# Kernel tuning notes

Hardware: AMD Instinct MI355X
Metric: run time of the kernel (lower is better)

Reference implementation:

```python
import jax, jax.numpy as jnp
import numpy as np

B, C, H, W = 16, 64, 64, 64
MID = max(1, C // 8)


def setup_inputs() -> dict:
    key = jax.random.key(0)
    k1, k2, k3, k4, k5 = jax.random.split(key, 5)
    x = jax.random.normal(k1, (B, C, H, W), dtype=jnp.float32)
    # 1x1 conv weights (spectral-norm conv collapses to a plain [out,in] matrix
    # with a scalar-normalized weight; we use the effective weight directly)
    Wq = jax.random.normal(k2, (MID, C), dtype=jnp.float32) * 0.05
    Wk = jax.random.normal(k3, (MID, C), dtype=jnp.float32) * 0.05
    Wv = jax.random.normal(k4, (C, C), dtype=jnp.float32) * 0.05
    gamma = jax.random.normal(k5, (1,), dtype=jnp.float32) * 0.1
    return {"x": x, "Wq": Wq, "Wk": Wk, "Wv": Wv, "gamma": gamma}


def reference(x, Wq, Wk, Wv, gamma):
    b, c, h, w = x.shape
    n = h * w
    mid = Wq.shape[0]
    xf = x.reshape(b, c, n)                      # [B,C,N]
    q = jnp.einsum('mc,bcn->bnm', Wq, xf)        # [B,N,mid]
    k = jnp.einsum('mc,bcn->bmn', Wk, xf)        # [B,mid,N]
    scale = np.float32(1.0 / np.sqrt(mid))       # torch: / q.size(-1)**0.5, q last dim = mid
    attn = jax.nn.softmax(jnp.einsum('bnm,bmk->bnk', q, k) * scale, axis=-1)  # [B,N,N]
    v = jnp.einsum('oc,bcn->bon', Wv, xf)        # [B,C,N]
    # torch: bmm(v, attn^T) -> out[b,c,j] = sum_n v[b,c,n] * attn[b,j,n]
    out = jnp.einsum('bon,bjn->boj', v, attn).reshape(b, c, h, w)
    return gamma * out + x
```

## Files before the change

### kernel.cpp

```cpp
#include <hip/hip_runtime.h>
#include <hip/hip_bf16.h>

#define BATCH 16
#define CC    64
#define NN    4096
#define MIDD  8

typedef __attribute__((ext_vector_type(8)))  short short8;
typedef __attribute__((ext_vector_type(16))) float f32x16;
typedef __attribute__((ext_vector_type(2)))  int   v2i;

static __device__ __forceinline__ ushort f2bf(float f) {
    return __bfloat16_as_ushort(__float2bfloat16(f));
}

static __device__ __forceinline__ void glds16(const void* g, void* l) {
    __builtin_amdgcn_global_load_lds(
        (const __attribute__((address_space(1))) unsigned int*)g,
        (__attribute__((address_space(3))) unsigned int*)l, 16, 0, 0);
}

static __device__ __forceinline__ unsigned cvt_pk(float lo, float hi) {
    unsigned r;
    asm("v_cvt_pk_bf16_f32 %0, %1, %2" : "=v"(r) : "v"(lo), "v"(hi));
    return r;
}

__global__ __launch_bounds__(256) void proj_kernel(
    const float* __restrict__ x,
    const float* __restrict__ Wq,
    const float* __restrict__ Wk,
    const float* __restrict__ Wv,
    ushort* __restrict__ qtr,
    ushort* __restrict__ ktr,
    ushort* __restrict__ v)
{
    __shared__ unsigned xT[64 * 32];

    int tid = threadIdx.x;
    int b   = blockIdx.x >> 6;
    int n0  = (blockIdx.x & 63) * 64;

    {
        int n  = tid & 63;
        int cp = tid >> 6;
        const float* xb = x + (size_t)b * CC * NN + n0 + n;
#pragma unroll
        for (int rep = 0; rep < 8; ++rep) {
            int c = cp * 2 + rep * 8;
            float a0 = xb[(size_t)c * NN];
            float a1 = xb[(size_t)(c + 1) * NN];
            int dwlog = cp + rep * 4;
            xT[n * 32 + (dwlog ^ (n & 31))] = cvt_pk(a0, a1);
        }
    }

    int wv   = tid >> 6;
    int lane = tid & 63;
    int hi   = lane >> 5;
    int r    = lane & 31;
    int s_   = wv & 1;
    bool hiT = wv >= 2;

    short8 wfa[4], wfb[4];
    if (!hiT) {
        const float* r0 = (r < 8)  ? (Wq + r * 64)
                        : (r < 16) ? (Wk + (r - 8) * 64)
                                   : (Wv + (r - 16) * 64);
        const float* r1 = Wv + (16 + r) * 64;
#pragma unroll
        for (int kc = 0; kc < 4; ++kc) {
            const float4* p0 = (const float4*)(r0 + kc * 16 + hi * 8);
            const float4* p1 = (const float4*)(r1 + kc * 16 + hi * 8);
            float4 a = p0[0], c4 = p0[1];
            float4 e = p1[0], g4 = p1[1];
            union { short8 s8; unsigned u[4]; } wa, wb;
            wa.u[0] = cvt_pk(a.x, a.y);  wa.u[1] = cvt_pk(a.z, a.w);
            wa.u[2] = cvt_pk(c4.x, c4.y); wa.u[3] = cvt_pk(c4.z, c4.w);
            wb.u[0] = cvt_pk(e.x, e.y);  wb.u[1] = cvt_pk(e.z, e.w);
            wb.u[2] = cvt_pk(g4.x, g4.y); wb.u[3] = cvt_pk(g4.z, g4.w);
            wfa[kc] = wa.s8; wfb[kc] = wb.s8;
        }
    } else {
        const float* r2 = Wv + (size_t)(r < 16 ? (48 + r) : 48) * 64;
        short8 z8 = {};
#pragma unroll
        for (int kc = 0; kc < 4; ++kc) {
            const float4* p2 = (const float4*)(r2 + kc * 16 + hi * 8);
            float4 a = p2[0], c4 = p2[1];
            union { short8 s8; unsigned u[4]; } wa;
            wa.u[0] = cvt_pk(a.x, a.y);  wa.u[1] = cvt_pk(a.z, a.w);
            wa.u[2] = cvt_pk(c4.x, c4.y); wa.u[3] = cvt_pk(c4.z, c4.w);
            wfa[kc] = (r < 16) ? wa.s8 : z8;
            wfb[kc] = z8;
        }
    }

    __syncthreads();

    short8 bf[4];
    int nr = s_ * 32 + r;
#pragma unroll
    for (int kc = 0; kc < 4; ++kc) {
        union { short8 s8; unsigned u[4]; } bu;
#pragma unroll
        for (int i = 0; i < 4; ++i) {
            int dwlog = kc * 8 + hi * 4 + i;
            bu.u[i] = xT[nr * 32 + (dwlog ^ r)];
        }
        bf[kc] = bu.s8;
    }

    int ng = n0 + s_ * 32 + r;
    size_t nb = (size_t)b * NN + ng;
    const float SCLQ = 0.35355339059327373f * 1.4426950408889634f;

    if (!hiT) {
        f32x16 acc = {};
#pragma unroll
        for (int kc = 0; kc < 4; ++kc)
            acc = __builtin_amdgcn_mfma_f32_32x32x16_bf16(wfa[kc], bf[kc], acc, 0, 0, 0);
        uint2 qd, kd, zd; zd.x = 0; zd.y = 0;
        qd.x = cvt_pk(acc[0] * SCLQ, acc[1] * SCLQ);
        qd.y = cvt_pk(acc[2] * SCLQ, acc[3] * SCLQ);
        kd.x = cvt_pk(acc[4], acc[5]);
        kd.y = cvt_pk(acc[6], acc[7]);
        *(uint2*)(qtr + nb * 8 + hi * 4) = qd;
        *(uint2*)(ktr + nb * 16 + hi * 4) = kd;
        *(uint2*)(ktr + nb * 16 + 8 + hi * 4) = zd;
#pragma unroll
        for (int reg = 8; reg < 16; ++reg) {
            int ch = (reg & 3) + 8 * ((reg >> 2) - 2) + 4 * hi;
            v[((size_t)b * CC + ch) * NN + ng] = f2bf(acc[reg]);
        }
        f32x16 ac1 = {};
#pragma unroll
        for (int kc = 0; kc < 4; ++kc)
            ac1 = __builtin_amdgcn_mfma_f32_32x32x16_bf16(wfb[kc], bf[kc], ac1, 0, 0, 0);
#pragma unroll
        for (int reg = 0; reg < 16; ++reg) {
            int ch = 16 + (reg & 3) + 8 * (reg >> 2) + 4 * hi;
            v[((size_t)b * CC + ch) * NN + ng] = f2bf(ac1[reg]);
        }
    } else {
        f32x16 acc = {};
#pragma unroll
        for (int kc = 0; kc < 4; ++kc)
            acc = __builtin_amdgcn_mfma_f32_32x32x16_bf16(wfa[kc], bf[kc], acc, 0, 0, 0);
#pragma unroll
        for (int reg = 0; reg < 8; ++reg) {
            int ch = 48 + (reg & 3) + 8 * (reg >> 2) + 4 * hi;
            v[((size_t)b * CC + ch) * NN + ng] = f2bf(acc[reg]);
        }
    }
}

__global__ __launch_bounds__(256, 2) void attn_kernel(
    const ushort* __restrict__ qtr,
    const ushort* __restrict__ ktr,
    const ushort* __restrict__ v,
    const float*  __restrict__ x,
    const float*  __restrict__ gamma,
    float* __restrict__ out)
{
    __shared__ __align__(16) char lds[3 * 10240];

    int bid = blockIdx.x;
    int wg  = (bid & 7) * 64 + (bid >> 3);
    int b   = wg >> 5;
    int qt  = wg & 31;

    int tid  = threadIdx.x;
    int wv   = tid >> 6;
    int lane = tid & 63;
    int hi   = lane >> 5;
    int ql   = lane & 31;
    int q0   = qt * 128 + wv * 32;

    short8 qf = *(const short8*)(qtr + ((size_t)b * NN + q0 + ql) * 8);
    float  gm = gamma[0];
    short8 zero8 = {};
    if (hi) qf = zero8;
    asm volatile("s_waitcnt vmcnt(0)" ::: "memory");

    const ushort* kb_ = ktr + (size_t)b * NN * 16;
    const ushort* vb_ = v   + (size_t)b * CC * NN;

    int oA = tid >> 3, sA = (tid & 7) ^ (oA & 7);
    int oB = oA + 32,  sB = (tid & 7) ^ (oB & 7);
    const ushort* vsrcA = vb_ + (size_t)oA * NN + sA * 8;
    const ushort* vsrcB = vb_ + (size_t)oB * NN + sB * 8;
    const ushort* ksrc0 = kb_ + (size_t)(tid & 63) * 16 + (tid >> 6) * 8;
    int vdA = tid * 16, vdB = (tid + 256) * 16, kd_ = 8192 + tid * 16;

    char* b0 = lds;
    char* b1 = lds + 10240;
    char* b2 = lds + 20480;

    union { short8 s8; ushort us[8]; } onesu;
#pragma unroll
    for (int i = 0; i < 8; ++i) onesu.us[i] = 0x3F80;
    short8 ones = onesu.s8;

    f32x16 zf   = {};
    f32x16 acc0 = {};
    f32x16 acc1 = {};
    f32x16 accl = {};

    glds16(vsrcA, b0 + vdA); glds16(vsrcB, b0 + vdB);
    if (wv < 2) glds16(ksrc0, b0 + kd_);
    glds16(vsrcA + 64, b1 + vdA); glds16(vsrcB + 64, b1 + vdB);
    if (wv < 2) glds16(ksrc0 + 64 * 16, b1 + kd_);

    for (int t = 0; t < 64; ++t) {
        int k2 = ((t + 2) & 63) * 64;

        __builtin_amdgcn_s_barrier();
        glds16(vsrcA + k2, b2 + vdA);
        glds16(vsrcB + k2, b2 + vdB);
        if (wv < 2) {
            glds16(ksrc0 + (size_t)k2 * 16, b2 + kd_);
            asm volatile("s_waitcnt vmcnt(6)" ::: "memory");
        } else {
            asm volatile("s_waitcnt vmcnt(4)" ::: "memory");
        }
        __builtin_amdgcn_s_barrier();
        __builtin_amdgcn_sched_barrier(0);

        short8 kf0 = *(const short8*)(b0 + 8192 + (hi * 64 + ql) * 16);
        short8 kf1 = *(const short8*)(b0 + 8192 + (hi * 64 + 32 + ql) * 16);

        short8 vA[2][2], vB[2][2];
#pragma unroll
        for (int c = 0; c < 2; ++c)
#pragma unroll
            for (int f = 0; f < 2; ++f) {
                int byteA = (ql * 8 + ((c * 4 + f * 2 + hi) ^ (ql & 7))) * 16;
                vA[c][f] = *(const short8*)(b0 + byteA);
                vB[c][f] = *(const short8*)(b0 + byteA + 4096);
            }

        f32x16 s0 = __builtin_amdgcn_mfma_f32_32x32x16_bf16(kf0, qf, zf, 0, 0, 0);
        f32x16 s1 = __builtin_amdgcn_mfma_f32_32x32x16_bf16(kf1, qf, zf, 0, 0, 0);

#pragma unroll
        for (int c = 0; c < 2; ++c) {
            const f32x16& s = c ? s1 : s0;
            float p[16];
#pragma unroll
            for (int r = 0; r < 16; ++r) p[r] = __builtin_amdgcn_exp2f(s[r]);

            unsigned u[8];
#pragma unroll
            for (int i = 0; i < 8; ++i) u[i] = cvt_pk(p[2 * i], p[2 * i + 1]);

            v2i r02 = __builtin_amdgcn_permlane32_swap(u[0], u[2], false, false);
            v2i r13 = __builtin_amdgcn_permlane32_swap(u[1], u[3], false, false);
            v2i r46 = __builtin_amdgcn_permlane32_swap(u[4], u[6], false, false);
            v2i r57 = __builtin_amdgcn_permlane32_swap(u[5], u[7], false, false);
            union { short8 s8; int i4[4]; } P0, P1;
            P0.i4[0] = r02.x; P0.i4[1] = r13.x; P0.i4[2] = r02.y; P0.i4[3] = r13.y;
            P1.i4[0] = r46.x; P1.i4[1] = r57.x; P1.i4[2] = r46.y; P1.i4[3] = r57.y;

            __builtin_amdgcn_s_setprio(1);
            acc0 = __builtin_amdgcn_mfma_f32_32x32x16_bf16(vA[c][0], P0.s8, acc0, 0, 0, 0);
            acc1 = __builtin_amdgcn_mfma_f32_32x32x16_bf16(vB[c][0], P0.s8, acc1, 0, 0, 0);
            accl = __builtin_amdgcn_mfma_f32_32x32x16_bf16(ones,    P0.s8, accl, 0, 0, 0);
            acc0 = __builtin_amdgcn_mfma_f32_32x32x16_bf16(vA[c][1], P1.s8, acc0, 0, 0, 0);
            acc1 = __builtin_amdgcn_mfma_f32_32x32x16_bf16(vB[c][1], P1.s8, acc1, 0, 0, 0);
            accl = __builtin_amdgcn_mfma_f32_32x32x16_bf16(ones,    P1.s8, accl, 0, 0, 0);
            __builtin_amdgcn_s_setprio(0);
        }

        char* tp = b0; b0 = b1; b1 = b2; b2 = tp;
    }

    float inv = gm / accl[0];

#pragma unroll
    for (int r = 0; r < 16; ++r) {
        int o = (r & 3) + 8 * (r >> 2) + 4 * hi;
        size_t i0 = ((size_t)(b * CC + o)) * NN + q0 + ql;
        out[i0] = acc0[r] * inv + x[i0];
        size_t i1 = i0 + (size_t)32 * NN;
        out[i1] = acc1[r] * inv + x[i1];
    }
}

extern "C" void kernel_launch(void* const* d_in, const int* in_sizes, int n_in,
                              void* d_out, int out_size, void* d_ws, size_t ws_size,
                              hipStream_t stream) {
    const float* x     = (const float*)d_in[0];
    const float* Wq    = (const float*)d_in[1];
    const float* Wk    = (const float*)d_in[2];
    const float* Wv    = (const float*)d_in[3];
    const float* gamma = (const float*)d_in[4];
    float* out = (float*)d_out;

    ushort* qtr = (ushort*)d_ws;
    ushort* ktr = qtr + (size_t)BATCH * NN * 8;
    ushort* vws = ktr + (size_t)BATCH * NN * 16;

    proj_kernel<<<dim3((BATCH * NN) / 64), dim3(256), 0, stream>>>(x, Wq, Wk, Wv, qtr, ktr, vws);
    attn_kernel<<<dim3((BATCH * NN) / 128), dim3(256), 0, stream>>>(qtr, ktr, vws, x, gamma, out);
}
```

Measured before the change: 144.3 us.

## Split attention key range across two wave groups with LDS reduction

Doubles the workgroup to 512 threads, with two halves of four waves each processing half of the key sequence for the same query tile, each using its own triple-buffered LDS region. Partial numerators and denominators from the second half are combined through LDS before the first half writes the output. K fragment loads are re-swizzled to avoid LDS bank conflicts, and V/K fragment reads are moved next to their use to reduce register pressure. This raises wave count per CU, at the cost of an extra reduction pass, a doubled LDS footprint, and a higher occupancy target of four blocks.

```diff
diff --git a/kernel.cpp b/kernel.cpp
--- a/kernel.cpp
+++ b/kernel.cpp
@@ -155,7 +155,7 @@
     }
 }
 
-__global__ __launch_bounds__(256, 2) void attn_kernel(
+__global__ __launch_bounds__(512, 4) void attn_kernel(
     const ushort* __restrict__ qtr,
     const ushort* __restrict__ ktr,
     const ushort* __restrict__ v,
@@ -163,7 +163,7 @@
     const float*  __restrict__ gamma,
     float* __restrict__ out)
 {
-    __shared__ __align__(16) char lds[3 * 10240];
+    __shared__ __align__(16) char lds[2 * 3 * 10240];
 
     int bid = blockIdx.x;
     int wg  = (bid & 7) * 64 + (bid >> 3);
@@ -172,10 +172,13 @@
 
     int tid  = threadIdx.x;
     int wv   = tid >> 6;
+    int qs   = wv & 3;
+    int h    = wv >> 2;
     int lane = tid & 63;
     int hi   = lane >> 5;
     int ql   = lane & 31;
-    int q0   = qt * 128 + wv * 32;
+    int q0   = qt * 128 + qs * 32;
+    int gt   = tid & 255;
 
     short8 qf = *(const short8*)(qtr + ((size_t)b * NN + q0 + ql) * 8);
     float  gm = gamma[0];
@@ -183,19 +186,26 @@
     if (hi) qf = zero8;
     asm volatile("s_waitcnt vmcnt(0)" ::: "memory");
 
-    const ushort* kb_ = ktr + (size_t)b * NN * 16;
-    const ushort* vb_ = v   + (size_t)b * CC * NN;
-
-    int oA = tid >> 3, sA = (tid & 7) ^ (oA & 7);
-    int oB = oA + 32,  sB = (tid & 7) ^ (oB & 7);
-    const ushort* vsrcA = vb_ + (size_t)oA * NN + sA * 8;
-    const ushort* vsrcB = vb_ + (size_t)oB * NN + sB * 8;
-    const ushort* ksrc0 = kb_ + (size_t)(tid & 63) * 16 + (tid >> 6) * 8;
-    int vdA = tid * 16, vdB = (tid + 256) * 16, kd_ = 8192 + tid * 16;
-
-    char* b0 = lds;
-    char* b1 = lds + 10240;
-    char* b2 = lds + 20480;
+    const ushort* kbh = ktr + (size_t)b * NN * 16 + (size_t)h * 2048 * 16;
+    const ushort* vbh = v   + (size_t)b * CC * NN + h * 2048;
+
+    int oA = gt >> 3, sA = (gt & 7) ^ (oA & 7);
+    int oB = oA + 32,  sB = (gt & 7) ^ (oB & 7);
+    const ushort* vsrcA = vbh + (size_t)oA * NN + sA * 8;
+    const ushort* vsrcB = vbh + (size_t)oB * NN + sB * 8;
+    int lk = gt ^ ((gt >> 3) & 7);
+    const ushort* ksrc0 = kbh + (size_t)(lk >> 1) * 16 + (lk & 1) * 8;
+
+    char* base = lds + h * 30720;
+    int vdA = gt * 16, vdB = (gt + 256) * 16, kd_ = 8192 + gt * 16;
+    char* b0 = base;
+    char* b1 = base + 10240;
+    char* b2 = base + 20480;
+
+    int L0 = ql * 2 + hi;
+    int L1 = (32 + ql) * 2 + hi;
+    int k0off = 8192 + (L0 ^ ((L0 >> 3) & 7)) * 16;
+    int k1off = 8192 + (L1 ^ ((L1 >> 3) & 7)) * 16;
 
     union { short8 s8; ushort us[8]; } onesu;
 #pragma unroll
@@ -208,17 +218,17 @@
     f32x16 accl = {};
 
     glds16(vsrcA, b0 + vdA); glds16(vsrcB, b0 + vdB);
-    if (wv < 2) glds16(ksrc0, b0 + kd_);
+    if (gt < 128) glds16(ksrc0, b0 + kd_);
     glds16(vsrcA + 64, b1 + vdA); glds16(vsrcB + 64, b1 + vdB);
-    if (wv < 2) glds16(ksrc0 + 64 * 16, b1 + kd_);
-
-    for (int t = 0; t < 64; ++t) {
-        int k2 = ((t + 2) & 63) * 64;
+    if (gt < 128) glds16(ksrc0 + 64 * 16, b1 + kd_);
+
+    for (int t = 0; t < 32; ++t) {
+        int k2 = ((t + 2) & 31) * 64;
 
         __builtin_amdgcn_s_barrier();
         glds16(vsrcA + k2, b2 + vdA);
         glds16(vsrcB + k2, b2 + vdB);
-        if (wv < 2) {
+        if (gt < 128) {
             glds16(ksrc0 + (size_t)k2 * 16, b2 + kd_);
             asm volatile("s_waitcnt vmcnt(6)" ::: "memory");
         } else {
@@ -227,25 +237,11 @@
         __builtin_amdgcn_s_barrier();
         __builtin_amdgcn_sched_barrier(0);
 
-        short8 kf0 = *(const short8*)(b0 + 8192 + (hi * 64 + ql) * 16);
-        short8 kf1 = *(const short8*)(b0 + 8192 + (hi * 64 + 32 + ql) * 16);
-
-        short8 vA[2][2], vB[2][2];
-#pragma unroll
-        for (int c = 0; c < 2; ++c)
-#pragma unroll
-            for (int f = 0; f < 2; ++f) {
-                int byteA = (ql * 8 + ((c * 4 + f * 2 + hi) ^ (ql & 7))) * 16;
-                vA[c][f] = *(const short8*)(b0 + byteA);
-                vB[c][f] = *(const short8*)(b0 + byteA + 4096);
-            }
-
-        f32x16 s0 = __builtin_amdgcn_mfma_f32_32x32x16_bf16(kf0, qf, zf, 0, 0, 0);
-        f32x16 s1 = __builtin_amdgcn_mfma_f32_32x32x16_bf16(kf1, qf, zf, 0, 0, 0);
-
 #pragma unroll
         for (int c = 0; c < 2; ++c) {
-            const f32x16& s = c ? s1 : s0;
+            short8 kf = *(const short8*)(b0 + (c ? k1off : k0off));
+            f32x16 s = __builtin_amdgcn_mfma_f32_32x32x16_bf16(kf, qf, zf, 0, 0, 0);
+
             float p[16];
 #pragma unroll
             for (int r = 0; r < 16; ++r) p[r] = __builtin_amdgcn_exp2f(s[r]);
@@ -262,28 +258,53 @@
             P0.i4[0] = r02.x; P0.i4[1] = r13.x; P0.i4[2] = r02.y; P0.i4[3] = r13.y;
             P1.i4[0] = r46.x; P1.i4[1] = r57.x; P1.i4[2] = r46.y; P1.i4[3] = r57.y;
 
+            int g0 = (ql * 8 + ((c * 4 + hi) ^ (ql & 7))) * 16;
+            int g1 = (ql * 8 + ((c * 4 + 2 + hi) ^ (ql & 7))) * 16;
+            short8 vA0 = *(const short8*)(b0 + g0);
+            short8 vB0 = *(const short8*)(b0 + g0 + 4096);
+            short8 vA1 = *(const short8*)(b0 + g1);
+            short8 vB1 = *(const short8*)(b0 + g1 + 4096);
+
             __builtin_amdgcn_s_setprio(1);
-            acc0 = __builtin_amdgcn_mfma_f32_32x32x16_bf16(vA[c][0], P0.s8, acc0, 0, 0, 0);
-            acc1 = __builtin_amdgcn_mfma_f32_32x32x16_bf16(vB[c][0], P0.s8, acc1, 0, 0, 0);
-            accl = __builtin_amdgcn_mfma_f32_32x32x16_bf16(ones,    P0.s8, accl, 0, 0, 0);
-            acc0 = __builtin_amdgcn_mfma_f32_32x32x16_bf16(vA[c][1], P1.s8, acc0, 0, 0, 0);
-            acc1 = __builtin_amdgcn_mfma_f32_32x32x16_bf16(vB[c][1], P1.s8, acc1, 0, 0, 0);
-            accl = __builtin_amdgcn_mfma_f32_32x32x16_bf16(ones,    P1.s8, accl, 0, 0, 0);
+            acc0 = __builtin_amdgcn_mfma_f32_32x32x16_bf16(vA0, P0.s8, acc0, 0, 0, 0);
+            acc1 = __builtin_amdgcn_mfma_f32_32x32x16_bf16(vB0, P0.s8, acc1, 0, 0, 0);
+            accl = __builtin_amdgcn_mfma_f32_32x32x16_bf16(ones, P0.s8, accl, 0, 0, 0);
+            acc0 = __builtin_amdgcn_mfma_f32_32x32x16_bf16(vA1, P1.s8, acc0, 0, 0, 0);
+            acc1 = __builtin_amdgcn_mfma_f32_32x32x16_bf16(vB1, P1.s8, acc1, 0, 0, 0);
+            accl = __builtin_amdgcn_mfma_f32_32x32x16_bf16(ones, P1.s8, accl, 0, 0, 0);
             __builtin_amdgcn_s_setprio(0);
         }
 
         char* tp = b0; b0 = b1; b1 = b2; b2 = tp;
     }
 
-    float inv = gm / accl[0];
-
-#pragma unroll
-    for (int r = 0; r < 16; ++r) {
-        int o = (r & 3) + 8 * (r >> 2) + 4 * hi;
-        size_t i0 = ((size_t)(b * CC + o)) * NN + q0 + ql;
-        out[i0] = acc0[r] * inv + x[i0];
-        size_t i1 = i0 + (size_t)32 * NN;
-        out[i1] = acc1[r] * inv + x[i1];
+    asm volatile("s_waitcnt vmcnt(0)" ::: "memory");
+    __syncthreads();
+
+    float* cl = (float*)lds;
+    if (h == 1) {
+#pragma unroll
+        for (int r = 0; r < 16; ++r) {
+            int ch = (r & 3) + 8 * (r >> 2) + 4 * hi;
+            cl[(qs * 64 + ch) * 32 + ql]      = acc0[r];
+            cl[(qs * 64 + 32 + ch) * 32 + ql] = acc1[r];
+        }
+        cl[8192 + qs * 32 + ql] = accl[0];
+    }
+    __syncthreads();
+    if (h == 0) {
+        float den = accl[0] + cl[8192 + qs * 32 + ql];
+        float inv = gm / den;
+#pragma unroll
+        for (int r = 0; r < 16; ++r) {
+            int ch = (r & 3) + 8 * (r >> 2) + 4 * hi;
+            float n0 = acc0[r] + cl[(qs * 64 + ch) * 32 + ql];
+            float n1 = acc1[r] + cl[(qs * 64 + 32 + ch) * 32 + ql];
+            size_t i0 = ((size_t)(b * CC + ch)) * NN + q0 + ql;
+            size_t i1 = i0 + (size_t)32 * NN;
+            out[i0] = n0 * inv + x[i0];
+            out[i1] = n1 * inv + x[i1];
+        }
     }
 }
 
@@ -302,5 +323,5 @@
     ushort* vws = ktr + (size_t)BATCH * NN * 16;
 
     proj_kernel<<<dim3((BATCH * NN) / 64), dim3(256), 0, stream>>>(x, Wq, Wk, Wv, qtr, ktr, vws);
-    attn_kernel<<<dim3((BATCH * NN) / 128), dim3(256), 0, stream>>>(qtr, ktr, vws, x, gamma, out);
-}
+    attn_kernel<<<dim3((BATCH * NN) / 128), dim3(512), 0, stream>>>(qtr, ktr, vws, x, gamma, out);
+}
```

Result: no change. 142.4 us (-1.4%).
